# Optimization experiments

Measured on AMD Instinct MI355X. Metric: run time of the kernel, lower is better.

Reference implementation:

```python
import jax, jax.numpy as jnp
import numpy as np

B, T, C, H = 4, 4096, 512, 64  # batch, seq(patches), n_embed, head_size

def setup_inputs() -> dict:
    key = jax.random.key(0)
    kx, kk, kq, kv = jax.random.split(key, 4)
    x = jax.random.normal(kx, (B, T, C), dtype=jnp.float32)
    # torch nn.Linear(n_embed, head_size).weight is [H, C]; store transposed [C, H]
    Wk = jax.random.normal(kk, (C, H), dtype=jnp.float32) / np.sqrt(C)
    Wq = jax.random.normal(kq, (C, H), dtype=jnp.float32) / np.sqrt(C)
    Wv = jax.random.normal(kv, (C, H), dtype=jnp.float32) / np.sqrt(C)
    return {"x": x, "Wk": Wk, "Wq": Wq, "Wv": Wv}

def reference(x, Wk, Wq, Wv):
    Bn, Tn, Cn = x.shape
    k = x @ Wk  # [B,T,H]
    q = x @ Wq
    v = x @ Wv
    # NOTE: original scales by C**-0.5 with C = n_embed (input dim), not head_size
    scores = jnp.einsum('bth,bsh->bts', q, k) * (Cn ** -0.5)  # [B,T,T]
    causal = jnp.tril(jnp.ones((Tn, Tn), dtype=bool))
    scores = jnp.where(causal, scores, -jnp.inf)
    attn = jax.nn.softmax(scores, axis=-1)
    return jnp.einsum('bts,bsh->bth', attn, v)  # [B,T,H]
```

## Files before the change

kernel.cpp:

```cpp
#include <hip/hip_runtime.h>
#include <hip/hip_bf16.h>

#define Bb 4
#define Tt 4096

typedef __bf16 bf16;
typedef __attribute__((ext_vector_type(8))) __bf16 bf16x8;
typedef __attribute__((ext_vector_type(4))) __bf16 bf16x4;
typedef __attribute__((ext_vector_type(4))) float f32x4;


__global__ __launch_bounds__(256) void wt_kernel(const float* __restrict__ Wk,
                                                 const float* __restrict__ Wq,
                                                 const float* __restrict__ Wv,
                                                 bf16* __restrict__ wt) {
  int idx = blockIdx.x * 256 + threadIdx.x;
  int mat = idx >> 15;
  int rem = idx & 32767;
  int n = rem >> 9;
  int k = rem & 511;
  const float* W = (mat == 0) ? Wk : (mat == 1) ? Wq : Wv;
  float v = W[k * 64 + n];
  if (mat == 1) v *= 0.044194173824159216f;
  wt[idx] = (bf16)v;
}

__global__ __launch_bounds__(256) void proj_kernel(const float* __restrict__ x,
                                                   const bf16* __restrict__ wt,
                                                   bf16* __restrict__ Kb,
                                                   bf16* __restrict__ Qb,
                                                   bf16* __restrict__ VTb) {
  __shared__ __attribute__((aligned(16))) bf16 xs[16][520];
  int tid = threadIdx.x;
  int row0 = blockIdx.x * 16;

  int sr = tid >> 4, sc = (tid & 15) * 4;
  const float* xr = x + (size_t)(row0 + sr) * 512;
#pragma unroll
  for (int j = 0; j < 8; ++j) {
    f32x4 a = *(const f32x4*)(xr + sc + j * 64);
    bf16x4 h;
#pragma unroll
    for (int e = 0; e < 4; ++e) h[e] = (bf16)a[e];
    *(bf16x4*)&xs[sr][sc + j * 64] = h;
  }
  __syncthreads();

  int wave = tid >> 6, lane = tid & 63, m = lane & 15, quad = lane >> 4;
  f32x4 acc[3];
#pragma unroll
  for (int i = 0; i < 3; ++i) acc[i] = (f32x4){0.f, 0.f, 0.f, 0.f};

#pragma unroll 4
  for (int kk = 0; kk < 512; kk += 32) {
    bf16x8 af = *(const bf16x8*)&xs[m][kk + quad * 8];
#pragma unroll
    for (int i = 0; i < 3; ++i) {
      int nt = wave * 3 + i;
      bf16x8 bfr = *(const bf16x8*)(wt + (nt >> 2) * 32768 +
                                    (((nt & 3) * 16) + m) * 512 + kk + quad * 8);
      acc[i] = __builtin_amdgcn_mfma_f32_16x16x32_bf16(af, bfr, acc[i], 0, 0, 0);
    }
  }

  int b = row0 >> 12, tloc = row0 & 4095;
#pragma unroll
  for (int i = 0; i < 3; ++i) {
    int nt = wave * 3 + i, mat = nt >> 2, n0 = (nt & 3) * 16;
    if (mat == 2) {
      bf16x4 pv;
#pragma unroll
      for (int r = 0; r < 4; ++r) pv[r] = (bf16)acc[i][r];
      *(bf16x4*)&VTb[((size_t)b * 64 + n0 + m) * 4096 + tloc + quad * 4] = pv;
    } else {
      bf16* dst = (mat == 0) ? Kb : Qb;
#pragma unroll
      for (int r = 0; r < 4; ++r)
        dst[(size_t)(row0 + quad * 4 + r) * 64 + n0 + m] = (bf16)acc[i][r];
    }
  }
}

__global__ __launch_bounds__(256) void attn_kernel(const bf16* __restrict__ Qb,
                                                   const bf16* __restrict__ Kb,
                                                   const bf16* __restrict__ VTb,
                                                   bf16* __restrict__ Opart,
                                                   float* __restrict__ Lpart,
                                                   float* __restrict__ out) {
  __shared__ __attribute__((aligned(16))) bf16 Kt[64][72];
  __shared__ __attribute__((aligned(16))) bf16 Vt[64][72];
  __shared__ __attribute__((aligned(16))) bf16 Pl[4][16][72];

  int tid = threadIdx.x, wave = tid >> 6, lane = tid & 63;
  int m = lane & 15, quad = lane >> 4, kq = quad * 8;

  int uu = 1151 - (int)blockIdx.x;
  int b = uu / 288, u2 = uu % 288;
  int g = 0;
  while (u2 >= 4 * (g + 1) * (g + 2)) ++g;
  int rr = u2 - 4 * g * (g + 1);
  int qi = 8 * g + rr / (g + 1);
  int c = rr % (g + 1);
  int t0 = qi * 64;
  int s_beg = c * 512;
  int s_end = min(s_beg + 512, t0 + 64);
  int niter = (s_end - s_beg) >> 6;

  const bf16* Qp = Qb + ((size_t)b * Tt + t0 + wave * 16 + m) * 64;
  bf16x8 aq0 = *(const bf16x8*)(Qp + kq);
  bf16x8 aq1 = *(const bf16x8*)(Qp + 32 + kq);

  bf16x8 onesb;
#pragma unroll
  for (int j = 0; j < 8; ++j) onesb[j] = (bf16)1.0f;

  f32x4 o[4];
#pragma unroll
  for (int i = 0; i < 4; ++i) o[i] = (f32x4){0.f, 0.f, 0.f, 0.f};
  f32x4 lsum = (f32x4){0.f, 0.f, 0.f, 0.f};

  int r_ = tid >> 2, seg = tid & 3;
  const bf16* Kbase = Kb + (size_t)b * Tt * 64;
  const bf16* VTbase = VTb + (size_t)b * 64 * 4096;

  const bf16* ks = Kbase + (size_t)(s_beg + r_) * 64 + seg * 16;
  bf16x8 k0 = *(const bf16x8*)ks;
  bf16x8 k1 = *(const bf16x8*)(ks + 8);
  const bf16* vs = VTbase + (size_t)r_ * 4096 + s_beg + seg * 16;
  bf16x8 v0 = *(const bf16x8*)vs;
  bf16x8 v1 = *(const bf16x8*)(vs + 8);

  for (int i = 0; i < niter; ++i) {
    int s0 = s_beg + i * 64;
    __syncthreads();
    *(bf16x8*)&Kt[r_][seg * 16] = k0;
    *(bf16x8*)&Kt[r_][seg * 16 + 8] = k1;
    *(bf16x8*)&Vt[r_][seg * 16] = v0;
    *(bf16x8*)&Vt[r_][seg * 16 + 8] = v1;
    __syncthreads();
    if (i + 1 < niter) {
      int sn = s0 + 64;
      const bf16* ks2 = Kbase + (size_t)(sn + r_) * 64 + seg * 16;
      k0 = *(const bf16x8*)ks2;
      k1 = *(const bf16x8*)(ks2 + 8);
      const bf16* vs2 = VTbase + (size_t)r_ * 4096 + sn + seg * 16;
      v0 = *(const bf16x8*)vs2;
      v1 = *(const bf16x8*)(vs2 + 8);
    }

    f32x4 s[4];
#pragma unroll
    for (int nt = 0; nt < 4; ++nt) {
      bf16x8 b0 = *(const bf16x8*)&Kt[nt * 16 + m][kq];
      bf16x8 b1 = *(const bf16x8*)&Kt[nt * 16 + m][32 + kq];
      f32x4 sa = (f32x4){0.f, 0.f, 0.f, 0.f};
      sa = __builtin_amdgcn_mfma_f32_16x16x32_bf16(aq0, b0, sa, 0, 0, 0);
      sa = __builtin_amdgcn_mfma_f32_16x16x32_bf16(aq1, b1, sa, 0, 0, 0);
      s[nt] = sa;
    }

    if (s0 + 64 > t0) {
#pragma unroll
      for (int nt = 0; nt < 4; ++nt) {
        int col = s0 + nt * 16 + m;
#pragma unroll
        for (int r = 0; r < 4; ++r) {
          int row = t0 + wave * 16 + quad * 4 + r;
          if (col > row) s[nt][r] = -1e30f;
        }
      }
    }

#pragma unroll
    for (int nt = 0; nt < 4; ++nt)
#pragma unroll
      for (int r = 0; r < 4; ++r)
        Pl[wave][quad * 4 + r][nt * 16 + m] = (bf16)__expf(s[nt][r]);

#pragma unroll
    for (int ch = 0; ch < 2; ++ch) {
      bf16x8 ap = *(const bf16x8*)&Pl[wave][m][ch * 32 + kq];
      lsum = __builtin_amdgcn_mfma_f32_16x16x32_bf16(ap, onesb, lsum, 0, 0, 0);
#pragma unroll
      for (int nt = 0; nt < 4; ++nt) {
        bf16x8 bv = *(const bf16x8*)&Vt[nt * 16 + m][ch * 32 + kq];
        o[nt] = __builtin_amdgcn_mfma_f32_16x16x32_bf16(ap, bv, o[nt], 0, 0, 0);
      }
    }
  }

  int rl0 = wave * 16 + quad * 4;
  if (qi < 8) {
    float* op = out + ((size_t)b * Tt + t0) * 64;
#pragma unroll
    for (int r = 0; r < 4; ++r) {
      float inv = 1.0f / lsum[r];
#pragma unroll
      for (int nt = 0; nt < 4; ++nt)
        op[(size_t)(rl0 + r) * 64 + nt * 16 + m] = o[nt][r] * inv;
    }
  } else {
    int p = b * 288 + 4 * g * (g + 1) + (qi - 8 * g) * (g + 1) + c;
    bf16* Op = Opart + (size_t)p * 4096;
#pragma unroll
    for (int r = 0; r < 4; ++r)
#pragma unroll
      for (int nt = 0; nt < 4; ++nt)
        Op[(rl0 + r) * 64 + nt * 16 + m] = (bf16)o[nt][r];
    if (m == 0) {
#pragma unroll
      for (int r = 0; r < 4; ++r) Lpart[p * 64 + rl0 + r] = lsum[r];
    }
  }
}

__global__ __launch_bounds__(256) void combine_kernel(const bf16* __restrict__ Opart,
                                                      const float* __restrict__ Lpart,
                                                      float* __restrict__ out) {
  int blk = blockIdx.x;
  int b = blk / 224, rem = blk % 224;
  int qi = 8 + (rem >> 2), rq = rem & 3;
  int g = qi >> 3, nc = g + 1;
  int pb = b * 288 + 4 * g * (g + 1) + (qi - 8 * g) * (g + 1);
  int t = threadIdx.x, col = t & 63, rl = t >> 6;
#pragma unroll
  for (int rr = 0; rr < 4; ++rr) {
    int row64 = rq * 16 + rl * 4 + rr;
    float L = 0.f, acc = 0.f;
    for (int cc = 0; cc < nc; ++cc) {
      L += Lpart[(pb + cc) * 64 + row64];
      acc += (float)Opart[(size_t)(pb + cc) * 4096 + row64 * 64 + col];
    }
    out[((size_t)b * Tt + qi * 64 + row64) * 64 + col] = acc / L;
  }
}

extern "C" void kernel_launch(void* const* d_in, const int* in_sizes, int n_in,
                              void* d_out, int out_size, void* d_ws, size_t ws_size,
                              hipStream_t stream) {
  const float* x = (const float*)d_in[0];
  const float* Wk = (const float*)d_in[1];
  const float* Wq = (const float*)d_in[2];
  const float* Wv = (const float*)d_in[3];
  float* out = (float*)d_out;

  char* w = (char*)d_ws;
  bf16* wt = (bf16*)w;
  bf16* Kb = (bf16*)(w + 196608);
  bf16* Qb = (bf16*)(w + 2293760);
  bf16* VTb = (bf16*)(w + 4390912);
  bf16* Opart = (bf16*)(w + 6488064);
  float* Lpart = (float*)(w + 15925248);

  wt_kernel<<<384, 256, 0, stream>>>(Wk, Wq, Wv, wt);
  proj_kernel<<<1024, 256, 0, stream>>>(x, wt, Kb, Qb, VTb);
  attn_kernel<<<1152, 256, 0, stream>>>(Qb, Kb, VTb, Opart, Lpart, out);
  combine_kernel<<<896, 256, 0, stream>>>(Opart, Lpart, out);
}
```

Baseline: 137.0 us.

## Double-buffer K/V tiles in LDS and reuse the spare K buffer for P

K and V tiles now live in two LDS buffers. The next tile is stored into the alternate buffer at the end of each iteration, which removes one __syncthreads per loop iteration. The per-wave P scratch is placed in the unused half of the next K buffer; each wave overwrites only its own rows there, so no extra barrier is needed for that reuse. A launch-bounds occupancy hint of 4 blocks is also added. The trade-off is a larger LDS footprint and more pressure on register allocation.

```diff
diff --git a/kernel.cpp b/kernel.cpp
--- a/kernel.cpp
+++ b/kernel.cpp
@@ -1,7 +1,6 @@
 #include <hip/hip_runtime.h>
 #include <hip/hip_bf16.h>
 
-#define Bb 4
 #define Tt 4096
 
 typedef __bf16 bf16;
@@ -81,18 +80,18 @@
   }
 }
 
-__global__ __launch_bounds__(256) void attn_kernel(const bf16* __restrict__ Qb,
-                                                   const bf16* __restrict__ Kb,
-                                                   const bf16* __restrict__ VTb,
-                                                   bf16* __restrict__ Opart,
-                                                   float* __restrict__ Lpart,
-                                                   float* __restrict__ out) {
-  __shared__ __attribute__((aligned(16))) bf16 Kt[64][72];
-  __shared__ __attribute__((aligned(16))) bf16 Vt[64][72];
-  __shared__ __attribute__((aligned(16))) bf16 Pl[4][16][72];
+__global__ __launch_bounds__(256, 4) void attn_kernel(const bf16* __restrict__ Qb,
+                                                      const bf16* __restrict__ Kb,
+                                                      const bf16* __restrict__ VTb,
+                                                      bf16* __restrict__ Opart,
+                                                      float* __restrict__ Lpart,
+                                                      float* __restrict__ out) {
+  __shared__ __attribute__((aligned(16))) bf16 Kt[2][64][72];
+  __shared__ __attribute__((aligned(16))) bf16 Vt[2][64][72];
 
   int tid = threadIdx.x, wave = tid >> 6, lane = tid & 63;
   int m = lane & 15, quad = lane >> 4, kq = quad * 8;
+  int r_ = tid >> 2, seg = tid & 3;
 
   int uu = 1151 - (int)blockIdx.x;
   int b = uu / 288, u2 = uu % 288;
@@ -103,8 +102,7 @@
   int c = rr % (g + 1);
   int t0 = qi * 64;
   int s_beg = c * 512;
-  int s_end = min(s_beg + 512, t0 + 64);
-  int niter = (s_end - s_beg) >> 6;
+  int niter = (min(s_beg + 512, t0 + 64) - s_beg) >> 6;
 
   const bf16* Qp = Qb + ((size_t)b * Tt + t0 + wave * 16 + m) * 64;
   bf16x8 aq0 = *(const bf16x8*)(Qp + kq);
@@ -119,31 +117,34 @@
   for (int i = 0; i < 4; ++i) o[i] = (f32x4){0.f, 0.f, 0.f, 0.f};
   f32x4 lsum = (f32x4){0.f, 0.f, 0.f, 0.f};
 
-  int r_ = tid >> 2, seg = tid & 3;
-  const bf16* Kbase = Kb + (size_t)b * Tt * 64;
-  const bf16* VTbase = VTb + (size_t)b * 64 * 4096;
-
-  const bf16* ks = Kbase + (size_t)(s_beg + r_) * 64 + seg * 16;
-  bf16x8 k0 = *(const bf16x8*)ks;
-  bf16x8 k1 = *(const bf16x8*)(ks + 8);
-  const bf16* vs = VTbase + (size_t)r_ * 4096 + s_beg + seg * 16;
-  bf16x8 v0 = *(const bf16x8*)vs;
-  bf16x8 v1 = *(const bf16x8*)(vs + 8);
-
+  const bf16* Kbase = Kb + (size_t)b * (Tt * 64);
+  const bf16* VTbase = VTb + (size_t)b * (64 * Tt);
+
+  {
+    const bf16* ks = Kbase + (size_t)(s_beg + r_) * 64 + seg * 16;
+    bf16x8 k0 = *(const bf16x8*)ks;
+    bf16x8 k1 = *(const bf16x8*)(ks + 8);
+    const bf16* vs = VTbase + (size_t)r_ * Tt + s_beg + seg * 16;
+    bf16x8 v0 = *(const bf16x8*)vs;
+    bf16x8 v1 = *(const bf16x8*)(vs + 8);
+    *(bf16x8*)&Kt[0][r_][seg * 16] = k0;
+    *(bf16x8*)&Kt[0][r_][seg * 16 + 8] = k1;
+    *(bf16x8*)&Vt[0][r_][seg * 16] = v0;
+    *(bf16x8*)&Vt[0][r_][seg * 16 + 8] = v1;
+  }
+
+  bf16x8 k0, k1, v0, v1;
   for (int i = 0; i < niter; ++i) {
     int s0 = s_beg + i * 64;
+    int cur = i & 1, nxt = cur ^ 1;
     __syncthreads();
-    *(bf16x8*)&Kt[r_][seg * 16] = k0;
-    *(bf16x8*)&Kt[r_][seg * 16 + 8] = k1;
-    *(bf16x8*)&Vt[r_][seg * 16] = v0;
-    *(bf16x8*)&Vt[r_][seg * 16 + 8] = v1;
-    __syncthreads();
+
     if (i + 1 < niter) {
       int sn = s0 + 64;
       const bf16* ks2 = Kbase + (size_t)(sn + r_) * 64 + seg * 16;
       k0 = *(const bf16x8*)ks2;
       k1 = *(const bf16x8*)(ks2 + 8);
-      const bf16* vs2 = VTbase + (size_t)r_ * 4096 + sn + seg * 16;
+      const bf16* vs2 = VTbase + (size_t)r_ * Tt + sn + seg * 16;
       v0 = *(const bf16x8*)vs2;
       v1 = *(const bf16x8*)(vs2 + 8);
     }
@@ -151,8 +152,8 @@
     f32x4 s[4];
 #pragma unroll
     for (int nt = 0; nt < 4; ++nt) {
-      bf16x8 b0 = *(const bf16x8*)&Kt[nt * 16 + m][kq];
-      bf16x8 b1 = *(const bf16x8*)&Kt[nt * 16 + m][32 + kq];
+      bf16x8 b0 = *(const bf16x8*)&Kt[cur][nt * 16 + m][kq];
+      bf16x8 b1 = *(const bf16x8*)&Kt[cur][nt * 16 + m][32 + kq];
       f32x4 sa = (f32x4){0.f, 0.f, 0.f, 0.f};
       sa = __builtin_amdgcn_mfma_f32_16x16x32_bf16(aq0, b0, sa, 0, 0, 0);
       sa = __builtin_amdgcn_mfma_f32_16x16x32_bf16(aq1, b1, sa, 0, 0, 0);
@@ -171,26 +172,34 @@
       }
     }
 
+    bf16(*Pl)[72] = &Kt[nxt][wave * 16];
 #pragma unroll
     for (int nt = 0; nt < 4; ++nt)
 #pragma unroll
       for (int r = 0; r < 4; ++r)
-        Pl[wave][quad * 4 + r][nt * 16 + m] = (bf16)__expf(s[nt][r]);
+        Pl[quad * 4 + r][nt * 16 + m] = (bf16)__expf(s[nt][r]);
 
 #pragma unroll
     for (int ch = 0; ch < 2; ++ch) {
-      bf16x8 ap = *(const bf16x8*)&Pl[wave][m][ch * 32 + kq];
+      bf16x8 ap = *(const bf16x8*)&Pl[m][ch * 32 + kq];
       lsum = __builtin_amdgcn_mfma_f32_16x16x32_bf16(ap, onesb, lsum, 0, 0, 0);
 #pragma unroll
       for (int nt = 0; nt < 4; ++nt) {
-        bf16x8 bv = *(const bf16x8*)&Vt[nt * 16 + m][ch * 32 + kq];
+        bf16x8 bv = *(const bf16x8*)&Vt[cur][nt * 16 + m][ch * 32 + kq];
         o[nt] = __builtin_amdgcn_mfma_f32_16x16x32_bf16(ap, bv, o[nt], 0, 0, 0);
       }
     }
+
+    if (i + 1 < niter) {
+      *(bf16x8*)&Kt[nxt][r_][seg * 16] = k0;
+      *(bf16x8*)&Kt[nxt][r_][seg * 16 + 8] = k1;
+      *(bf16x8*)&Vt[nxt][r_][seg * 16] = v0;
+      *(bf16x8*)&Vt[nxt][r_][seg * 16 + 8] = v1;
+    }
   }
 
   int rl0 = wave * 16 + quad * 4;
-  if (qi < 8) {
+  if (g == 0) {
     float* op = out + ((size_t)b * Tt + t0) * 64;
 #pragma unroll
     for (int r = 0; r < 4; ++r) {
```

After: 138.5 us. Within noise of the previous version (+1.0%).
